# Kernel tuning notes

Measured on AMD Instinct MI355X. Metric: run time of the kernel, lower is better.

## Reference

```python
import jax, jax.numpy as jnp
import numpy as np

B, S, D, H = 2, 2048, 2048, 16
HD = D // H  # 128
ROPE_BASE = 10000.0


def _rope_tables(seq_len, head_dim, dtype=jnp.float32):
    inv_freq = 1.0 / (ROPE_BASE ** (jnp.arange(0, head_dim, 2, dtype=jnp.float32) / head_dim))
    t = jnp.arange(seq_len, dtype=jnp.float32)
    freqs = jnp.outer(t, inv_freq)  # [S, HD/2]
    # broadcast shape [1, S, 1, HD/2]
    return jnp.cos(freqs)[None, :, None, :].astype(dtype), jnp.sin(freqs)[None, :, None, :].astype(dtype)


def _apply_rope(x, cos, sin):
    # x: [B, S, H, HD]; interleaved split, output concatenated by halves (matches torch code)
    x1 = x[..., ::2]
    x2 = x[..., 1::2]
    return jnp.concatenate([x1 * cos - x2 * sin, x1 * sin + x2 * cos], axis=-1)


def setup_inputs() -> dict:
    key = jax.random.key(0)
    ks = jax.random.split(key, 9)
    xavier = lambda k: jax.random.uniform(k, (D, D), jnp.float32, -1.0, 1.0) * np.sqrt(6.0 / (D + D))
    return {
        "x": jax.random.normal(ks[0], (B, S, D), jnp.float32),
        "attention_mask": jnp.ones((B, S), jnp.int32),
        "wq": xavier(ks[1]), "bq": jnp.zeros((D,), jnp.float32),
        "wk": xavier(ks[2]), "bk": jnp.zeros((D,), jnp.float32),
        "wv": xavier(ks[3]), "bv": jnp.zeros((D,), jnp.float32),
        "wo": xavier(ks[4]), "bo": jnp.zeros((D,), jnp.float32),
    }


def reference(x, attention_mask, wq, bq, wk, bk, wv, bv, wo, bo):
    b, s, _ = x.shape
    scale = HD ** -0.5
    q = (x @ wq + bq).reshape(b, s, H, HD)
    k = (x @ wk + bk).reshape(b, s, H, HD)
    v = (x @ wv + bv).reshape(b, s, H, HD)
    cos, sin = _rope_tables(s, HD, x.dtype)
    q = _apply_rope(q, cos, sin)
    k = _apply_rope(k, cos, sin)
    # [B, H, S, S]
    scores = jnp.einsum('bqhd,bkhd->bhqk', q, k) * scale
    mask = attention_mask[:, None, None, :]  # 2D mask -> [B,1,1,S]
    scores = jnp.where(mask == 0, jnp.asarray(-1e9, scores.dtype), scores)
    attn = jax.nn.softmax(scores, axis=-1)
    out = jnp.einsum('bhqk,bkhd->bqhd', attn, v).reshape(b, s, D)
    return out @ wo + bo
```

## Files before the change

### kernel.cpp

```cpp
#include <hip/hip_runtime.h>

#define Bc 2
#define Sc 2048
#define Dc 2048
#define Hc 16
#define HDc 128
#define Mc 4096

typedef __bf16 bf16_t;
typedef __bf16 bf16x4 __attribute__((ext_vector_type(4)));
typedef __bf16 bf16x8 __attribute__((ext_vector_type(8)));
typedef float f32x4 __attribute__((ext_vector_type(4)));
typedef float f32x16 __attribute__((ext_vector_type(16)));

__device__ __forceinline__ f32x4 mfma16(bf16x8 a, bf16x8 b, f32x4 c) {
  return __builtin_amdgcn_mfma_f32_16x16x32_bf16(a, b, c, 0, 0, 0);
}
__device__ __forceinline__ f32x16 mfma32(bf16x8 a, bf16x8 b, f32x16 c) {
  return __builtin_amdgcn_mfma_f32_32x32x16_bf16(a, b, c, 0, 0, 0);
}

typedef const unsigned __attribute__((address_space(1))) gu32_t;
typedef unsigned __attribute__((address_space(3))) lu32_t;

__device__ __forceinline__ void gload_lds16(const void* g, void* l) {
  gu32_t* gp = (gu32_t*)(unsigned long long)g;
  lu32_t* lp = (lu32_t*)(unsigned)(unsigned long long)l;
  __builtin_amdgcn_global_load_lds(gp, lp, 16, 0, 0);
}

__device__ __forceinline__ unsigned cvtpk(float lo, float hi_) {
  unsigned r;
  asm("v_cvt_pk_bf16_f32 %0, %1, %2" : "=v"(r) : "v"(lo), "v"(hi_));
  return r;
}
__device__ __forceinline__ void plswap(unsigned& a, unsigned& b) {
  asm volatile("v_permlane32_swap_b32 %0, %1" : "+v"(a), "+v"(b));
}

__global__ void cvt_bf16_kernel(const float* __restrict__ in, bf16_t* __restrict__ out, int n4) {
  int i = blockIdx.x * blockDim.x + threadIdx.x;
  if (i < n4) {
    float4 v = ((const float4*)in)[i];
    bf16x4 o;
    o[0] = (bf16_t)v.x; o[1] = (bf16_t)v.y; o[2] = (bf16_t)v.z; o[3] = (bf16_t)v.w;
    ((bf16x4*)out)[i] = o;
  }
}

__global__ void transpose_cvt_kernel(const float* __restrict__ w, bf16_t* __restrict__ wt) {
  __shared__ float tile[32][33];
  const int tx = threadIdx.x, ty = threadIdx.y;
  const int n0 = blockIdx.x * 32, k0 = blockIdx.y * 32;
#pragma unroll
  for (int i = 0; i < 32; i += 8)
    tile[ty + i][tx] = w[(size_t)(k0 + ty + i) * Dc + n0 + tx];
  __syncthreads();
#pragma unroll
  for (int i = 0; i < 32; i += 8)
    wt[(size_t)(n0 + ty + i) * Dc + k0 + tx] = (bf16_t)tile[tx][ty + i];
}

template <int MODE, int NT8>
__global__ __launch_bounds__(512, 1) void gemmp_kernel(
    const bf16_t* __restrict__ A, const bf16_t* __restrict__ Bt,
    const float* __restrict__ bias0, const float* __restrict__ bias1,
    const float* __restrict__ bias2,
    void* __restrict__ out0, void* __restrict__ out1, void* __restrict__ out2) {
  __shared__ __align__(16) bf16_t sA[3][256 * 64];
  __shared__ __align__(16) bf16_t sB[3][128 * 64];
  const int tid = threadIdx.x;
  const int lane = tid & 63, wid = tid >> 6;
  const int l15 = lane & 15, g = lane >> 4;
  const int wrow = wid >> 1, wcol = wid & 1;

  const int nwg = 16 * NT8, cpx = nwg / 8;
  const int wgid = ((int)blockIdx.x & 7) * cpx + ((int)blockIdx.x >> 3);
  const int nt = wgid % NT8, mt = wgid / NT8;
  const int m0 = mt * 256, n0 = nt * 128;

  const bf16_t* Ab = A + (size_t)m0 * 2048;
  const bf16_t* Bb = Bt + (size_t)n0 * 2048;

#define GP_STAGE_A(kt, i_)                                           \
  {                                                                  \
    int s_ = (i_) * 512 + tid;                                       \
    int r_ = s_ >> 3;                                                \
    int c_ = ((s_ & 7) ^ (r_ & 7)) * 8;                              \
    gload_lds16(Ab + (size_t)r_ * 2048 + (kt) * 64 + c_,             \
                (char*)&sA[(kt) % 3][0] + s_ * 16);                  \
  }
#define GP_STAGE_B(kt, i_)                                           \
  {                                                                  \
    int s_ = (i_) * 512 + tid;                                       \
    int r_ = s_ >> 3;                                                \
    int c_ = ((s_ & 7) ^ (r_ & 7)) * 8;                              \
    gload_lds16(Bb + (size_t)r_ * 2048 + (kt) * 64 + c_,             \
                (char*)&sB[(kt) % 3][0] + s_ * 16);                  \
  }

  f32x4 acc[4][4] = {};

  GP_STAGE_A(0, 0) GP_STAGE_A(0, 1) GP_STAGE_A(0, 2) GP_STAGE_A(0, 3)
  GP_STAGE_B(0, 0) GP_STAGE_B(0, 1)
  GP_STAGE_A(1, 0) GP_STAGE_A(1, 1) GP_STAGE_A(1, 2) GP_STAGE_A(1, 3)
  GP_STAGE_B(1, 0) GP_STAGE_B(1, 1)

#define GP_BODY(t, DOSTG, VMSTR)                                               \
  {                                                                            \
    asm volatile("s_waitcnt vmcnt(" VMSTR ")" ::: "memory");                   \
    __builtin_amdgcn_s_barrier();       \
    __builtin_amdgcn_sched_barrier(0);                                         \
    const char* pA = (const char*)&sA[(t) % 3][0];                             \
    const char* pB = (const char*)&sB[(t) % 3][0];                             \
    bf16x8 af[4][2], bf0[2][2], bf1[2][2];                                     \
    _Pragma("unroll") for (int mi = 0; mi < 4; ++mi)                           \
        _Pragma("unroll") for (int ks = 0; ks < 2; ++ks) {                     \
      int r = wrow * 64 + mi * 16 + l15;                                       \
      af[mi][ks] = *(const bf16x8*)(pA + r * 128 + (((ks * 4 + g) ^ (r & 7)) * 16)); \
    }                                                                          \
    _Pragma("unroll") for (int ni = 0; ni < 2; ++ni)                           \
        _Pragma("unroll") for (int ks = 0; ks < 2; ++ks) {                     \
      int r = wcol * 64 + ni * 16 + l15;                                       \
      bf0[ni][ks] = *(const bf16x8*)(pB + r * 128 + (((ks * 4 + g) ^ (r & 7)) * 16)); \
    }                                                                          \
    if (DOSTG) { GP_STAGE_A((t) + 2, 0) GP_STAGE_A((t) + 2, 1) GP_STAGE_B((t) + 2, 0) } \
    __builtin_amdgcn_s_setprio(1);                                             \
    _Pragma("unroll") for (int mi = 0; mi < 4; ++mi)                           \
        _Pragma("unroll") for (int ni = 0; ni < 2; ++ni)                       \
            _Pragma("unroll") for (int ks = 0; ks < 2; ++ks)                   \
                acc[mi][ni] = mfma16(af[mi][ks], bf0[ni][ks], acc[mi][ni]);    \
    __builtin_amdgcn_s_setprio(0);                                             \
    __builtin_amdgcn_s_barrier();                           \
    __builtin_amdgcn_sched_barrier(0);                                         \
    _Pragma("unroll") for (int ni = 0; ni < 2; ++ni)                           \
        _Pragma("unroll") for (int ks = 0; ks < 2; ++ks) {                     \
      int r = wcol * 64 + (ni + 2) * 16 + l15;                                 \
      bf1[ni][ks] = *(const bf16x8*)(pB + r * 128 + (((ks * 4 + g) ^ (r & 7)) * 16)); \
    }                                                                          \
    if (DOSTG) { GP_STAGE_A((t) + 2, 2) GP_STAGE_A((t) + 2, 3) GP_STAGE_B((t) + 2, 1) } \
    __builtin_amdgcn_s_setprio(1);                                             \
    _Pragma("unroll") for (int mi = 0; mi < 4; ++mi)                           \
        _Pragma("unroll") for (int ni = 0; ni < 2; ++ni)                       \
            _Pragma("unroll") for (int ks = 0; ks < 2; ++ks)                   \
                acc[mi][ni + 2] = mfma16(af[mi][ks], bf1[ni][ks], acc[mi][ni + 2]); \
    __builtin_amdgcn_s_setprio(0);                                             \
  }

  for (int t = 0; t < 30; ++t) GP_BODY(t, 1, "6");
  GP_BODY(30, 0, "6");
  GP_BODY(31, 0, "0");

#undef GP_BODY
#undef GP_STAGE_A
#undef GP_STAGE_B

#pragma unroll
  for (int mi = 0; mi < 4; ++mi) {
#pragma unroll
    for (int ni = 0; ni < 4; ++ni) {
      const int ncol = n0 + wcol * 64 + ni * 16 + l15;
      if (MODE == 2) {
        const float bv = bias0[ncol];
#pragma unroll
        for (int r = 0; r < 4; ++r) {
          const int mrow = m0 + wrow * 64 + mi * 16 + g * 4 + r;
          ((float*)out0)[(size_t)mrow * 2048 + ncol] = acc[mi][ni][r] + bv;
        }
      } else {
        const int proj = ncol >> 11, nloc = ncol & 2047;
        const float* bp = proj == 0 ? bias0 : (proj == 1 ? bias1 : bias2);
        bf16_t* op = (bf16_t*)(proj == 0 ? out0 : (proj == 1 ? out1 : out2));
        const float bv = bp[nloc];
        const int h = nloc >> 7, hd = nloc & 127;
#pragma unroll
        for (int r = 0; r < 4; ++r) {
          const int mrow = m0 + wrow * 64 + mi * 16 + g * 4 + r;
          const int b = mrow >> 11, sq = mrow & 2047;
          const float v = acc[mi][ni][r] + bv;
          if (proj < 2)
            op[(((size_t)(b * Hc + h) * Sc + sq) * HDc) + hd] = (bf16_t)v;
          else
            op[(((size_t)(b * Hc + h) * HDc + hd) * Sc) + sq] = (bf16_t)v;
        }
      }
    }
  }
}

__global__ __launch_bounds__(256) void rope_kernel(bf16_t* __restrict__ qk) {
  const int w = threadIdx.x >> 6, lane = threadIdx.x & 63;
  const long row = (long)blockIdx.x * 4 + w;
  const int s = (int)(row & (Sc - 1));
  bf16_t* p = qk + row * HDc;
  float x1 = (float)p[2 * lane];
  float x2 = (float)p[2 * lane + 1];
  float freq = expf(-(float)lane * (9.210340371976184f / 64.0f));
  float ang = (float)s * freq;
  float sn, cs;
  sincosf(ang, &sn, &cs);
  __syncthreads();
  p[lane] = (bf16_t)(x1 * cs - x2 * sn);
  p[lane + 64] = (bf16_t)(x1 * sn + x2 * cs);
}

__global__ __launch_bounds__(256, 2) void attn_kernel(
    const bf16_t* __restrict__ Q, const bf16_t* __restrict__ Kr,
    const bf16_t* __restrict__ Vt, const int* __restrict__ mask,
    bf16_t* __restrict__ AO) {
  __shared__ __align__(16) bf16_t sK[2][64 * 128];
  __shared__ __align__(16) bf16_t sV[2][64 * 128];
  __shared__ float mbias[Sc];
  __shared__ float bcast[4][32];
  const int tid = threadIdx.x;
  const int w = tid >> 6, lane = tid & 63;
  const int l31 = lane & 31, hi = lane >> 5;
  const int wbase = w * 64;

  const int bid = blockIdx.x;
  const int L = ((bid & 7) << 6) + (bid >> 3);
  const int qc = L & 15, h = (L >> 4) & 15, b = L >> 8;

  const int* mb = mask + b * Sc;
#pragma unroll
  for (int i = 0; i < Sc / 256; ++i)
    mbias[i * 256 + tid] = mb[i * 256 + tid] ? 0.f : -1e9f;

  const int q0 = qc * 128 + w * 32;
  const bf16_t* qb = Q + ((size_t)(b * Hc + h) * Sc + q0) * HDc;
  const bf16_t* kb = Kr + ((size_t)(b * Hc + h) * Sc) * HDc;
  const bf16_t* vb = Vt + ((size_t)(b * Hc + h) * HDc) * Sc;

  bf16x8 qf[8];
  {
    const bf16_t* qr = qb + (size_t)l31 * HDc + hi * 8;
#pragma unroll
    for (int kk = 0; kk < 8; ++kk) qf[kk] = *(const bf16x8*)(qr + kk * 16);
  }

#define STAGE_KV(sKb, sVb, kv0_)                                             \
  {                                                                          \
    _Pragma("unroll") for (int p = 0; p < 4; ++p) {                          \
      int s_ = p * 256 + tid;                                                \
      int rk = s_ >> 4, ck = s_ & 15;                                        \
      gload_lds16(kb + (size_t)((kv0_) + rk) * HDc + ((ck ^ (rk & 15)) * 8), \
                  (char*)(sKb) + (size_t)(p * 256 + wbase) * 16);            \
      int d63 = s_ >> 4, sv = s_ & 15;                                       \
      int tmp = sv ^ (d63 & 15);                                             \
      int hb = tmp >> 3, cv = tmp & 7;                                       \
      gload_lds16(vb + (size_t)(hb * 64 + d63) * Sc + (kv0_) + cv * 8,       \
                  (char*)(sVb) + (size_t)(p * 256 + wbase) * 16);            \
    }                                                                        \
  }

  bf16_t* sKc = &sK[0][0];
  bf16_t* sKn = &sK[1][0];
  bf16_t* sVc = &sV[0][0];
  bf16_t* sVn = &sV[1][0];

  STAGE_KV(sKc, sVc, 0);
  asm volatile("s_waitcnt vmcnt(0)" ::: "memory");
  __syncthreads();

  f32x16 acc[4];
#pragma unroll
  for (int d = 0; d < 4; ++d) acc[d] = 0.f;
  float mrun = -3.0e38f, lrun = 0.f;
  const float scale = 0.08838834764831845f;

  for (int kv0 = 0; kv0 < Sc; kv0 += 64) {
    if (kv0 + 64 < Sc) STAGE_KV(sKn, sVn, kv0 + 64);

    f32x16 s0 = 0.f, s1 = 0.f;
    {
      const char* kbase = (const char*)sKc;
      __builtin_amdgcn_s_setprio(1);
#pragma unroll
      for (int kk = 0; kk < 8; ++kk) {
        bf16x8 k0f = *(const bf16x8*)(kbase + l31 * 256 + (((2 * kk + hi) ^ (l31 & 15)) * 16));
        bf16x8 k1f = *(const bf16x8*)(kbase + (32 + l31) * 256 + (((2 * kk + hi) ^ ((32 + l31) & 15)) * 16));
        s0 = mfma32(k0f, qf[kk], s0);
        s1 = mfma32(k1f, qf[kk], s1);
      }
      __builtin_amdgcn_s_setprio(0);
    }
    float v[32];
    {
      const float* mp = mbias + kv0 + 4 * hi;
#pragma unroll
      for (int g4 = 0; g4 < 4; ++g4) {
        f32x4 b0 = *(const f32x4*)(mp + 8 * g4);
        f32x4 b1 = *(const f32x4*)(mp + 32 + 8 * g4);
#pragma unroll
        for (int j = 0; j < 4; ++j) {
          v[g4 * 4 + j] = s0[g4 * 4 + j] * scale + b0[j];
          v[16 + g4 * 4 + j] = s1[g4 * 4 + j] * scale + b1[j];
        }
      }
    }
    float tm = v[0];
#pragma unroll
    for (int r = 1; r < 32; ++r) tm = fmaxf(tm, v[r]);
    tm = fmaxf(tm, __shfl_xor(tm, 32));
    if (__any(tm > mrun + 8.f)) {
      float mnew = fmaxf(mrun, tm);
      float al = __expf(mrun - mnew);
      mrun = mnew;
      lrun *= al;
      bcast[w][l31] = al;
      asm volatile("s_waitcnt lgkmcnt(0)" ::: "memory");
      __builtin_amdgcn_sched_barrier(0);
#pragma unroll
      for (int g4 = 0; g4 < 4; ++g4) {
        f32x4 alr = *(const f32x4*)(&bcast[w][8 * g4 + 4 * hi]);
#pragma unroll
        for (int dblk = 0; dblk < 4; ++dblk)
#pragma unroll
          for (int j = 0; j < 4; ++j) acc[dblk][g4 * 4 + j] *= alr[j];
      }
    }
    float ts = 0.f;
#pragma unroll
    for (int r = 0; r < 32; ++r) {
      v[r] = __expf(v[r] - mrun);
      ts += v[r];
    }
    ts += __shfl_xor(ts, 32);
    lrun += ts;
    unsigned pk[4][4];
#pragma unroll
    for (int ks = 0; ks < 4; ++ks) {
      unsigned a1 = cvtpk(v[ks * 8 + 0], v[ks * 8 + 1]);
      unsigned b1 = cvtpk(v[ks * 8 + 4], v[ks * 8 + 5]);
      unsigned a2 = cvtpk(v[ks * 8 + 2], v[ks * 8 + 3]);
      unsigned b2 = cvtpk(v[ks * 8 + 6], v[ks * 8 + 7]);
      plswap(a1, b1);
      plswap(a2, b2);
      pk[ks][0] = a1; pk[ks][1] = a2; pk[ks][2] = b1; pk[ks][3] = b2;
    }
    {
      const char* vbase = (const char*)sVc;
      __builtin_amdgcn_s_setprio(1);
#pragma unroll
      for (int ks = 0; ks < 4; ++ks) {
        bf16x8 pa = *(const bf16x8*)&pk[ks][0];
#pragma unroll
        for (int dblk = 0; dblk < 4; ++dblk) {
          int d = dblk * 32 + l31;
          int slot = (((d >> 6) * 8 + (2 * ks + hi)) ^ (d & 15));
          bf16x8 vf = *(const bf16x8*)(vbase + (d & 63) * 256 + slot * 16);
          acc[dblk] = mfma32(pa, vf, acc[dblk]);
        }
      }
      __builtin_amdgcn_s_setprio(0);
    }
    asm volatile("s_waitcnt vmcnt(0)" ::: "memory");
    __syncthreads();
    bf16_t* t1 = sKc; sKc = sKn; sKn = t1;
    bf16_t* t2 = sVc; sVc = sVn; sVn = t2;
  }

  float inv = 1.f / lrun;
  bcast[w][l31] = inv;
  asm volatile("s_waitcnt lgkmcnt(0)" ::: "memory");
  __builtin_amdgcn_sched_barrier(0);
  bf16_t* ob = AO + ((size_t)b * Sc + q0) * Dc + h * HDc;
#pragma unroll
  for (int g4 = 0; g4 < 4; ++g4) {
    f32x4 ir = *(const f32x4*)(&bcast[w][8 * g4 + 4 * hi]);
#pragma unroll
    for (int j = 0; j < 4; ++j) {
      int q = 8 * g4 + 4 * hi + j;
#pragma unroll
      for (int dblk = 0; dblk < 4; ++dblk)
        ob[(size_t)q * Dc + dblk * 32 + l31] = (bf16_t)(acc[dblk][g4 * 4 + j] * ir[j]);
    }
  }
}

#define MB(x) ((size_t)(x) << 20)

extern "C" void kernel_launch(void* const* d_in, const int* in_sizes, int n_in,
                              void* d_out, int out_size, void* d_ws, size_t ws_size,
                              hipStream_t stream) {
  const float* x = (const float*)d_in[0];
  const int* mask = (const int*)d_in[1];
  const float* wq = (const float*)d_in[2];
  const float* bq = (const float*)d_in[3];
  const float* wk = (const float*)d_in[4];
  const float* bk = (const float*)d_in[5];
  const float* wv = (const float*)d_in[6];
  const float* bv = (const float*)d_in[7];
  const float* wo = (const float*)d_in[8];
  const float* bo = (const float*)d_in[9];
  float* out = (float*)d_out;

  char* ws = (char*)d_ws;
  bf16_t* xb     = (bf16_t*)(ws + MB(0));
  bf16_t* wqkvT  = (bf16_t*)(ws + MB(16));
  bf16_t* woT    = (bf16_t*)(ws + MB(40));
  bf16_t* qbuf   = (bf16_t*)(ws + MB(48));
  bf16_t* kbuf   = (bf16_t*)(ws + MB(64));
  bf16_t* vtb    = (bf16_t*)(ws + MB(80));
  bf16_t* ao     = (bf16_t*)(ws + MB(96));

  cvt_bf16_kernel<<<8192, 256, 0, stream>>>(x, xb, (Mc * Dc) / 4);

  dim3 tg(64, 64), tb(32, 8);
  transpose_cvt_kernel<<<tg, tb, 0, stream>>>(wq, wqkvT);
  transpose_cvt_kernel<<<tg, tb, 0, stream>>>(wk, wqkvT + (size_t)Dc * Dc);
  transpose_cvt_kernel<<<tg, tb, 0, stream>>>(wv, wqkvT + 2 * (size_t)Dc * Dc);
  transpose_cvt_kernel<<<tg, tb, 0, stream>>>(wo, woT);

  gemmp_kernel<0, 48><<<768, 512, 0, stream>>>(xb, wqkvT, bq, bk, bv, qbuf, kbuf, vtb);

  rope_kernel<<<(2 * Bc * Hc * Sc) / 4, 256, 0, stream>>>(qbuf);

  attn_kernel<<<Bc * Hc * (Sc / 128), 256, 0, stream>>>(qbuf, kbuf, vtb, mask, ao);

  gemmp_kernel<2, 16><<<256, 512, 0, stream>>>(ao, woT, bo, bo, bo, out, out, out);
}
```

Measured before the change: 299.9 us.

## Fuse RoPE into QKV GEMM epilogue and merge weight-transpose launches

Removes the separate RoPE kernel: the QKV projection epilogue now rotates Q and K in registers before storing. It pairs adjacent columns with a lane xor-shuffle and reads cos/sin from a small table built by a new kernel. This skips a full read-modify-write pass over the Q and K buffers. The rotated pairs are stored at their interleaved positions rather than as concatenated halves, which leaves the attention dot product unchanged because Q and K get the same permutation. The four weight transpose/convert launches are also merged into one launch using a z-dimension; the cost is extra epilogue work and table loads inside the GEMM.

```diff
diff --git a/kernel.cpp b/kernel.cpp
--- a/kernel.cpp
+++ b/kernel.cpp
@@ -48,8 +48,22 @@
   }
 }
 
-__global__ void transpose_cvt_kernel(const float* __restrict__ w, bf16_t* __restrict__ wt) {
+__global__ void rope_table_kernel(float2* __restrict__ tbl) {
+  const int s = blockIdx.x, j = threadIdx.x;
+  float freq = expf(-(float)j * (9.210340371976184f / 64.0f));
+  float ang = (float)s * freq;
+  float sn, cs;
+  sincosf(ang, &sn, &cs);
+  tbl[s * 64 + j] = make_float2(cs, sn);
+}
+
+__global__ void transpose_cvt4_kernel(const float* __restrict__ w0, const float* __restrict__ w1,
+                                      const float* __restrict__ w2, const float* __restrict__ w3,
+                                      bf16_t* __restrict__ dqkv, bf16_t* __restrict__ dwo) {
   __shared__ float tile[32][33];
+  const int z = blockIdx.z;
+  const float* w = z == 0 ? w0 : (z == 1 ? w1 : (z == 2 ? w2 : w3));
+  bf16_t* wt = z < 3 ? dqkv + (size_t)z * Dc * Dc : dwo;
   const int tx = threadIdx.x, ty = threadIdx.y;
   const int n0 = blockIdx.x * 32, k0 = blockIdx.y * 32;
 #pragma unroll
@@ -65,7 +79,7 @@
 __global__ __launch_bounds__(512, 1) void gemmp_kernel(
     const bf16_t* __restrict__ A, const bf16_t* __restrict__ Bt,
     const float* __restrict__ bias0, const float* __restrict__ bias1,
-    const float* __restrict__ bias2,
+    const float* __restrict__ bias2, const float2* __restrict__ tbl,
     void* __restrict__ out0, void* __restrict__ out1, void* __restrict__ out2) {
   __shared__ __align__(16) bf16_t sA[3][256 * 64];
   __shared__ __align__(16) bf16_t sB[3][128 * 64];
@@ -109,7 +123,7 @@
 #define GP_BODY(t, DOSTG, VMSTR)                                               \
   {                                                                            \
     asm volatile("s_waitcnt vmcnt(" VMSTR ")" ::: "memory");                   \
-    __builtin_amdgcn_s_barrier();       \
+    __builtin_amdgcn_s_barrier();                                              \
     __builtin_amdgcn_sched_barrier(0);                                         \
     const char* pA = (const char*)&sA[(t) % 3][0];                             \
     const char* pB = (const char*)&sB[(t) % 3][0];                             \
@@ -131,7 +145,7 @@
             _Pragma("unroll") for (int ks = 0; ks < 2; ++ks)                   \
                 acc[mi][ni] = mfma16(af[mi][ks], bf0[ni][ks], acc[mi][ni]);    \
     __builtin_amdgcn_s_setprio(0);                                             \
-    __builtin_amdgcn_s_barrier();                           \
+    __builtin_amdgcn_s_barrier();                                              \
     __builtin_amdgcn_sched_barrier(0);                                         \
     _Pragma("unroll") for (int ni = 0; ni < 2; ++ni)                           \
         _Pragma("unroll") for (int ks = 0; ks < 2; ++ks) {                     \
@@ -155,53 +169,57 @@
 #undef GP_STAGE_A
 #undef GP_STAGE_B
 
-#pragma unroll
-  for (int mi = 0; mi < 4; ++mi) {
-#pragma unroll
-    for (int ni = 0; ni < 4; ++ni) {
-      const int ncol = n0 + wcol * 64 + ni * 16 + l15;
-      if (MODE == 2) {
+  if (MODE == 2) {
+#pragma unroll
+    for (int mi = 0; mi < 4; ++mi) {
+#pragma unroll
+      for (int ni = 0; ni < 4; ++ni) {
+        const int ncol = n0 + wcol * 64 + ni * 16 + l15;
         const float bv = bias0[ncol];
 #pragma unroll
         for (int r = 0; r < 4; ++r) {
           const int mrow = m0 + wrow * 64 + mi * 16 + g * 4 + r;
           ((float*)out0)[(size_t)mrow * 2048 + ncol] = acc[mi][ni][r] + bv;
         }
-      } else {
-        const int proj = ncol >> 11, nloc = ncol & 2047;
-        const float* bp = proj == 0 ? bias0 : (proj == 1 ? bias1 : bias2);
-        bf16_t* op = (bf16_t*)(proj == 0 ? out0 : (proj == 1 ? out1 : out2));
+      }
+    }
+  } else {
+    const int proj = n0 >> 11;
+    const float* bp = proj == 0 ? bias0 : (proj == 1 ? bias1 : bias2);
+    bf16_t* op = (bf16_t*)(proj == 0 ? out0 : (proj == 1 ? out1 : out2));
+#pragma unroll
+    for (int mi = 0; mi < 4; ++mi) {
+#pragma unroll
+      for (int ni = 0; ni < 4; ++ni) {
+        const int ncol = n0 + wcol * 64 + ni * 16 + l15;
+        const int nloc = ncol & 2047;
         const float bv = bp[nloc];
         const int h = nloc >> 7, hd = nloc & 127;
-#pragma unroll
-        for (int r = 0; r < 4; ++r) {
-          const int mrow = m0 + wrow * 64 + mi * 16 + g * 4 + r;
-          const int b = mrow >> 11, sq = mrow & 2047;
-          const float v = acc[mi][ni][r] + bv;
-          if (proj < 2)
-            op[(((size_t)(b * Hc + h) * Sc + sq) * HDc) + hd] = (bf16_t)v;
-          else
+        if (proj < 2) {
+          const int j = hd >> 1;
+#pragma unroll
+          for (int r = 0; r < 4; ++r) {
+            const int mrow = m0 + wrow * 64 + mi * 16 + g * 4 + r;
+            const int b = mrow >> 11, sq = mrow & 2047;
+            float vv = acc[mi][ni][r] + bv;
+            float part = __shfl_xor(vv, 1);
+            float2 cn = tbl[(size_t)sq * 64 + j];
+            float ov = (l15 & 1) ? (part * cn.y + vv * cn.x)
+                                 : (vv * cn.x - part * cn.y);
+            op[(((size_t)(b * Hc + h) * Sc + sq) * HDc) + hd] = (bf16_t)ov;
+          }
+        } else {
+#pragma unroll
+          for (int r = 0; r < 4; ++r) {
+            const int mrow = m0 + wrow * 64 + mi * 16 + g * 4 + r;
+            const int b = mrow >> 11, sq = mrow & 2047;
+            const float v = acc[mi][ni][r] + bv;
             op[(((size_t)(b * Hc + h) * HDc + hd) * Sc) + sq] = (bf16_t)v;
+          }
         }
       }
     }
   }
-}
-
-__global__ __launch_bounds__(256) void rope_kernel(bf16_t* __restrict__ qk) {
-  const int w = threadIdx.x >> 6, lane = threadIdx.x & 63;
-  const long row = (long)blockIdx.x * 4 + w;
-  const int s = (int)(row & (Sc - 1));
-  bf16_t* p = qk + row * HDc;
-  float x1 = (float)p[2 * lane];
-  float x2 = (float)p[2 * lane + 1];
-  float freq = expf(-(float)lane * (9.210340371976184f / 64.0f));
-  float ang = (float)s * freq;
-  float sn, cs;
-  sincosf(ang, &sn, &cs);
-  __syncthreads();
-  p[lane] = (bf16_t)(x1 * cs - x2 * sn);
-  p[lane + 64] = (bf16_t)(x1 * sn + x2 * cs);
 }
 
 __global__ __launch_bounds__(256, 2) void attn_kernel(
@@ -403,20 +421,17 @@
   bf16_t* kbuf   = (bf16_t*)(ws + MB(64));
   bf16_t* vtb    = (bf16_t*)(ws + MB(80));
   bf16_t* ao     = (bf16_t*)(ws + MB(96));
+  float2* rtbl   = (float2*)(ws + MB(112));
 
   cvt_bf16_kernel<<<8192, 256, 0, stream>>>(x, xb, (Mc * Dc) / 4);
-
-  dim3 tg(64, 64), tb(32, 8);
-  transpose_cvt_kernel<<<tg, tb, 0, stream>>>(wq, wqkvT);
-  transpose_cvt_kernel<<<tg, tb, 0, stream>>>(wk, wqkvT + (size_t)Dc * Dc);
-  transpose_cvt_kernel<<<tg, tb, 0, stream>>>(wv, wqkvT + 2 * (size_t)Dc * Dc);
-  transpose_cvt_kernel<<<tg, tb, 0, stream>>>(wo, woT);
-
-  gemmp_kernel<0, 48><<<768, 512, 0, stream>>>(xb, wqkvT, bq, bk, bv, qbuf, kbuf, vtb);
-
-  rope_kernel<<<(2 * Bc * Hc * Sc) / 4, 256, 0, stream>>>(qbuf);
+  rope_table_kernel<<<Sc, 64, 0, stream>>>(rtbl);
+
+  dim3 tg(64, 64, 4), tb(32, 8);
+  transpose_cvt4_kernel<<<tg, tb, 0, stream>>>(wq, wk, wv, wo, wqkvT, woT);
+
+  gemmp_kernel<0, 48><<<768, 512, 0, stream>>>(xb, wqkvT, bq, bk, bv, rtbl, qbuf, kbuf, vtb);
 
   attn_kernel<<<Bc * Hc * (Sc / 128), 256, 0, stream>>>(qbuf, kbuf, vtb, mask, ao);
 
-  gemmp_kernel<2, 16><<<256, 512, 0, stream>>>(ao, woT, bo, bo, bo, out, out, out);
-}
+  gemmp_kernel<2, 16><<<256, 512, 0, stream>>>(ao, woT, bo, bo, bo, rtbl, out, out, out);
+}
```

Result: faster. 270.3 us (-9.8%).
